# Kernel optimization log

Hardware: AMD Instinct MI355X
Metric: run time of the kernel (lower is better)

Reference implementation:

```python
import jax, jax.numpy as jnp
import numpy as np

ROPE_BASE = 10000.0

def rope_tables(n, r):
    inv = 1.0 / (ROPE_BASE ** (jnp.arange(0, r, 2, dtype=jnp.float32) / r))  # [r/2]
    ang = jnp.arange(n, dtype=jnp.float32)[:, None] * inv[None, :]           # [n, r/2]
    cos = jnp.concatenate([jnp.cos(ang), jnp.cos(ang)], axis=-1)             # [n, r]
    sin = jnp.concatenate([jnp.sin(ang), jnp.sin(ang)], axis=-1)
    return cos, sin

def apply_rope(x, cos, sin):
    # x: [B, H, T, r]; cos/sin: [T, r]
    half = x.shape[-1] // 2
    x_rot = jnp.concatenate([-x[..., half:], x[..., :half]], axis=-1)
    return x * cos + x_rot * sin

def setup_inputs() -> dict:
    key = jax.random.key(0)
    ks = jax.random.split(key, 8)
    B, S, L = 2, 1024, 1024
    dim_q, h, k, d_c, d_cq, r = 2048, 16, 128, 512, 1536, 64
    w = 0.02  # weight scale to keep activations numerically tame
    return {
        'hidden_q': jax.random.normal(ks[0], (B, S, dim_q), jnp.float32),
        'kv_c':     jax.random.normal(ks[1], (B, L, d_c), jnp.float32),
        'Wq':       jax.random.normal(ks[2], (h * k, dim_q), jnp.float32) * w,
        'w_kc_q':   jax.random.normal(ks[3], (h, k, d_cq), jnp.float32) * w,
        'W_qr':     jax.random.normal(ks[4], (h, d_cq, r), jnp.float32) * (w / np.sqrt(r)),
        'W_kr':     jax.random.normal(ks[5], (h, d_c, r), jnp.float32) * w,
        'w_kc_kv':  jax.random.normal(ks[6], (h, k, d_c), jnp.float32) * w,
        'Wo':       jax.random.normal(ks[7], (dim_q, h * k), jnp.float32) * w,
    }

def reference(hidden_q, kv_c, Wq, w_kc_q, W_qr, W_kr, w_kc_kv, Wo):
    B, S, _ = hidden_q.shape
    L = kv_c.shape[1]
    h, k, _ = w_kc_q.shape
    r = W_qr.shape[-1]
    # q projection: [B,S,h,k]
    q_hk = (hidden_q @ Wq.T).reshape(B, S, h, k)
    # low-rank expand to q-compressed space then retrieval space
    q_big = jnp.einsum('bshk,hkq->bshq', q_hk, w_kc_q)          # [B,S,h,d_cq]
    q_r = jnp.einsum('bshq,hqr->bhsr', q_big, W_qr)             # [B,h,S,r]
    k_r = jnp.einsum('bld,hdr->bhlr', kv_c, W_kr)               # [B,h,L,r]
    cos_S, sin_S = rope_tables(S, r)
    cos_L, sin_L = rope_tables(L, r)
    q_r = apply_rope(q_r, cos_S, sin_S)
    k_r = apply_rope(k_r, cos_L, sin_L)
    # attention in retrieval space, values are compressed kv (shared across heads)
    scores = jnp.einsum('bhsr,bhlr->bhsl', q_r, k_r)            # scale baked into W_qr
    attn = jax.nn.softmax(scores, axis=-1)
    ctx_c = jnp.einsum('bhsl,bld->bhsd', attn, kv_c)            # [B,h,S,d_c]
    # decompress per head: w_kc_kv is [h,k,d_c]
    ctx_lat = jnp.einsum('bhsd,hkd->bshk', ctx_c, w_kc_kv).reshape(B, S, h * k)
    return ctx_lat @ Wo.T
```

## Files before the change

kernel.cpp:

```cpp
#include <hip/hip_runtime.h>
#include <math.h>
#include <stdint.h>


typedef __attribute__((ext_vector_type(8))) short short8;
typedef __attribute__((ext_vector_type(4))) float f32x4;

#define GLOAD16(gsrc, ldst)                                                            \
  __builtin_amdgcn_global_load_lds((const __attribute__((address_space(1))) void*)(gsrc), \
                                   (__attribute__((address_space(3))) void*)(ldst), 16, 0, 0)

__device__ inline uint16_t f2b(float x) {
  uint32_t u = __builtin_bit_cast(uint32_t, x);
  u += 0x7fff + ((u >> 16) & 1);
  return (uint16_t)(u >> 16);
}
__device__ inline float b2f(uint16_t b) {
  uint32_t u = ((uint32_t)b) << 16;
  return __builtin_bit_cast(float, u);
}
__device__ inline uint32_t cvtpk_bf16(float lo, float hi) {
  uint32_t d;
  asm("v_cvt_pk_bf16_f32 %0, %1, %2" : "=v"(d) : "v"(lo), "v"(hi));
  return d;
}

__global__ __launch_bounds__(256) void prep_kernel(
    const float* __restrict__ s0, uint16_t* __restrict__ t0, const float* __restrict__ s1,
    uint16_t* __restrict__ t1, const float* __restrict__ s2, uint16_t* __restrict__ t2,
    const float* __restrict__ s3, uint16_t* __restrict__ t3, const float* __restrict__ s4,
    uint16_t* __restrict__ t4, float* __restrict__ cosK, float* __restrict__ sinK,
    float* __restrict__ cosQ, float* __restrict__ sinQ, const float* __restrict__ Wq,
    uint16_t* __restrict__ WqT, const float* __restrict__ W_qr, uint16_t* __restrict__ WqrT,
    const float* __restrict__ W_kr, uint16_t* __restrict__ WkrT) {
  __shared__ float t[32][33];
  int bid = blockIdx.x;
  if (bid >= 6912) {
    int tb = bid - 6912;
    const float* src;
    uint16_t* dst;
    int R, C, r0, c0;
    if (tb < 4096) {
      src = Wq; dst = WqT; R = 2048; C = 2048;
      r0 = (tb & 63) * 32; c0 = (tb >> 6) * 32;
    } else if (tb < 5632) {
      int b = tb - 4096;
      int z = b / 96, rem = b % 96;
      src = W_qr + (size_t)z * 98304; dst = WqrT + (size_t)z * 98304;
      R = 1536; C = 64;
      r0 = (rem >> 1) * 32; c0 = (rem & 1) * 32;
    } else {
      int b = tb - 5632;
      int z = b / 32, rem = b % 32;
      src = W_kr + (size_t)z * 32768; dst = WkrT + (size_t)z * 32768;
      R = 512; C = 64;
      r0 = (rem >> 1) * 32; c0 = (rem & 1) * 32;
    }
    int tr = threadIdx.x >> 5, tc = threadIdx.x & 31;
#pragma unroll
    for (int i = 0; i < 4; ++i) t[tr + i * 8][tc] = src[(size_t)(r0 + tr + i * 8) * C + c0 + tc];
    __syncthreads();
#pragma unroll
    for (int i = 0; i < 4; ++i)
      dst[(size_t)(c0 + tr + i * 8) * R + r0 + tc] = f2b(t[tc][tr + i * 8]);
    return;
  }
  if (bid >= 6656) {
    const float LOG2E = 1.44269504088896341f;
    int idx = (bid - 6656) * 256 + threadIdx.x;
    int s = idx >> 6, j = idx & 63;
    int i = j & 31;
    float inv = powf(10000.0f, -(float)(2 * i) / 64.0f);
    float ang = (float)s * inv;
    float c = cosf(ang), sn = sinf(ang);
    cosK[idx] = c;
    sinK[idx] = sn;
    cosQ[idx] = c * LOG2E;
    sinQ[idx] = sn * LOG2E;
    return;
  }
  const float* s;
  uint16_t* tt;
  int off;
  if (bid < 2048) { s = s0; tt = t0; off = bid; }
  else if (bid < 2560) { s = s1; tt = t1; off = bid - 2048; }
  else if (bid < 3072) { s = s2; tt = t2; off = bid - 2560; }
  else if (bid < 5120) { s = s3; tt = t3; off = bid - 3072; }
  else { s = s4; tt = t4; off = bid - 5120; }
  int i = off * 256 + threadIdx.x;
  const float4* s4v = (const float4*)s;
  float4 a = s4v[i * 2], b = s4v[i * 2 + 1];
  union {
    uint16_t u[8];
    uint4 v;
  } o;
  o.u[0] = f2b(a.x); o.u[1] = f2b(a.y); o.u[2] = f2b(a.z); o.u[3] = f2b(a.w);
  o.u[4] = f2b(b.x); o.u[5] = f2b(b.y); o.u[6] = f2b(b.z); o.u[7] = f2b(b.w);
  ((uint4*)tt)[i] = o.v;
}

template <int BM, int EPI, int SPLITK = 1>
__global__ __launch_bounds__(256) void gemm_mfma_kernel(const uint16_t* __restrict__ A,
                                                        const uint16_t* __restrict__ Bt,
                                                        void* __restrict__ Cv, int K, int lda,
                                                        int ldb, int ldc, int aZ, int bZ,
                                                        int cZ) {
  constexpr int MT = BM / 32;
  __shared__ __align__(16) uint16_t As[2][BM * 64];
  __shared__ __align__(16) uint16_t Bs[2][128 * 64];
  int z = blockIdx.z;
  if (SPLITK > 1) {
    int zh = z / SPLITK, zk = z % SPLITK;
    A += (size_t)zh * aZ + (size_t)zk * K;
    Bt += (size_t)zh * bZ + (size_t)zk * K;
  } else {
    A += (size_t)z * aZ;
    Bt += (size_t)z * bZ;
  }
  int m0 = blockIdx.x * BM, n0 = blockIdx.y * 128;
  int tid = threadIdx.x;
  int wave = tid >> 6, lane = tid & 63;
  int wm = wave >> 1, wn = wave & 1;
  int rS = lane >> 3, sl = lane & 7;
  int lr = lane >> 4, lc = lane & 15;

  auto stage = [&](int k0, int buf) {
#pragma unroll
    for (int i = 0; i < MT; ++i) {
      int idx = wave * MT + i;
      int row = idx * 8 + rS;
      GLOAD16(A + (size_t)(m0 + row) * lda + k0 + ((sl ^ (row & 7)) << 3),
              (uint8_t*)As[buf] + idx * 1024);
    }
#pragma unroll
    for (int i = 0; i < 4; ++i) {
      int idx = wave * 4 + i;
      int row = idx * 8 + rS;
      GLOAD16(Bt + (size_t)(n0 + row) * ldb + k0 + ((sl ^ (row & 7)) << 3),
              (uint8_t*)Bs[buf] + idx * 1024);
    }
  };

  f32x4 acc[MT][4] = {};
  stage(0, 0);
  int cur = 0;
  for (int k0 = 0; k0 < K; k0 += 64) {
    __syncthreads();
    if (k0 + 64 < K) stage(k0 + 64, cur ^ 1);
    short8 af[MT][2], bf[4][2];
#pragma unroll
    for (int t = 0; t < MT; ++t)
#pragma unroll
      for (int ks = 0; ks < 2; ++ks) {
        int slot = ks * 4 + lr;
        int ra = wm * (BM / 2) + t * 16 + lc;
        af[t][ks] =
            *(const short8*)((const uint8_t*)As[cur] + ra * 128 + ((slot ^ (ra & 7)) << 4));
      }
#pragma unroll
    for (int t = 0; t < 4; ++t)
#pragma unroll
      for (int ks = 0; ks < 2; ++ks) {
        int slot = ks * 4 + lr;
        int rb = wn * 64 + t * 16 + lc;
        bf[t][ks] =
            *(const short8*)((const uint8_t*)Bs[cur] + rb * 128 + ((slot ^ (rb & 7)) << 4));
      }
    __builtin_amdgcn_s_setprio(1);
#pragma unroll
    for (int mt = 0; mt < MT; ++mt)
#pragma unroll
      for (int nt = 0; nt < 4; ++nt) {
        acc[mt][nt] =
            __builtin_amdgcn_mfma_f32_16x16x32_bf16(af[mt][0], bf[nt][0], acc[mt][nt], 0, 0, 0);
        acc[mt][nt] =
            __builtin_amdgcn_mfma_f32_16x16x32_bf16(af[mt][1], bf[nt][1], acc[mt][nt], 0, 0, 0);
      }
    __builtin_amdgcn_s_setprio(0);
    cur ^= 1;
  }
#pragma unroll
  for (int mt = 0; mt < MT; ++mt)
#pragma unroll
    for (int nt = 0; nt < 4; ++nt)
#pragma unroll
      for (int r = 0; r < 4; ++r) {
        int m = m0 + wm * (BM / 2) + mt * 16 + lr * 4 + r;
        int n = n0 + wn * 64 + nt * 16 + lc;
        float v = acc[mt][nt][r];
        if (EPI == 0)
          ((float*)Cv)[(size_t)z * cZ + (size_t)m * ldc + n] = v;
        else
          ((uint16_t*)Cv)[(size_t)z * cZ + (size_t)m * ldc + n] = f2b(v);
      }
}

__global__ __launch_bounds__(256) void fold2_kernel(const float* __restrict__ tmp1,
                                                    const uint16_t* __restrict__ WqT,
                                                    uint16_t* __restrict__ WfoldT) {
  __shared__ __align__(16) uint16_t As[2][64 * 64];
  __shared__ __align__(16) uint16_t Bs[2][128 * 64];
  int z = blockIdx.z;
  int n0 = blockIdx.y * 128;
  const uint16_t* Bt = WqT + z * 128;
  int tid = threadIdx.x;
  int wave = tid >> 6, lane = tid & 63;
  int wm = wave >> 1, wn = wave & 1;
  int rS = lane >> 3, sl = lane & 7;
  int lr = lane >> 4, lc = lane & 15;

  {
    int row = tid >> 2;
    int kbase = (tid & 3) * 32;
    const float* tp = tmp1 + (size_t)z * 32768 + row * 128;
#pragma unroll
    for (int c = 0; c < 8; ++c) {
      int k4 = kbase + c * 4;
      float4 s = *(const float4*)(tp + k4);
      float4 s1 = *(const float4*)(tp + 8192 + k4);
      float4 s2 = *(const float4*)(tp + 16384 + k4);
      float4 s3 = *(const float4*)(tp + 24576 + k4);
      s.x = ((s.x + s1.x) + s2.x) + s3.x;
      s.y = ((s.y + s1.y) + s2.y) + s3.y;
      s.z = ((s.z + s1.z) + s2.z) + s3.z;
      s.w = ((s.w + s1.w) + s2.w) + s3.w;
      uint32_t lo = cvtpk_bf16(s.x, s.y);
      uint32_t hi = cvtpk_bf16(s.z, s.w);
      int buf = k4 >> 6, kl = k4 & 63;
      int slot = kl >> 3;
      uint32_t addr = row * 128 + ((slot ^ (row & 7)) << 4) + (kl & 7) * 2;
      *(uint32_t*)((uint8_t*)As[buf] + addr) = lo;
      *(uint32_t*)((uint8_t*)As[buf] + addr + 4) = hi;
    }
  }

  auto stageB = [&](int k0, int buf) {
#pragma unroll
    for (int i = 0; i < 4; ++i) {
      int idx = wave * 4 + i;
      int row = idx * 8 + rS;
      GLOAD16(Bt + (size_t)(n0 + row) * 2048 + k0 + ((sl ^ (row & 7)) << 3),
              (uint8_t*)Bs[buf] + idx * 1024);
    }
  };

  f32x4 acc[2][4] = {};
  stageB(0, 0);
  int cur = 0;
  for (int k0 = 0; k0 < 128; k0 += 64) {
    __syncthreads();
    if (k0 + 64 < 128) stageB(64, 1);
    short8 af[2][2], bf[4][2];
#pragma unroll
    for (int t = 0; t < 2; ++t)
#pragma unroll
      for (int ks = 0; ks < 2; ++ks) {
        int slot = ks * 4 + lr;
        int ra = wm * 32 + t * 16 + lc;
        af[t][ks] =
            *(const short8*)((const uint8_t*)As[cur] + ra * 128 + ((slot ^ (ra & 7)) << 4));
      }
#pragma unroll
    for (int t = 0; t < 4; ++t)
#pragma unroll
      for (int ks = 0; ks < 2; ++ks) {
        int slot = ks * 4 + lr;
        int rb = wn * 64 + t * 16 + lc;
        bf[t][ks] =
            *(const short8*)((const uint8_t*)Bs[cur] + rb * 128 + ((slot ^ (rb & 7)) << 4));
      }
    __builtin_amdgcn_s_setprio(1);
#pragma unroll
    for (int mt = 0; mt < 2; ++mt)
#pragma unroll
      for (int nt = 0; nt < 4; ++nt) {
        acc[mt][nt] =
            __builtin_amdgcn_mfma_f32_16x16x32_bf16(af[mt][0], bf[nt][0], acc[mt][nt], 0, 0, 0);
        acc[mt][nt] =
            __builtin_amdgcn_mfma_f32_16x16x32_bf16(af[mt][1], bf[nt][1], acc[mt][nt], 0, 0, 0);
      }
    __builtin_amdgcn_s_setprio(0);
    cur ^= 1;
  }
#pragma unroll
  for (int mt = 0; mt < 2; ++mt)
#pragma unroll
    for (int nt = 0; nt < 4; ++nt)
#pragma unroll
      for (int r = 0; r < 4; ++r) {
        int m = wm * 32 + mt * 16 + lr * 4 + r;
        int n = n0 + wn * 64 + nt * 16 + lc;
        WfoldT[(size_t)z * 131072 + (size_t)m * 2048 + n] = f2b(acc[mt][nt][r]);
      }
}

__global__ __launch_bounds__(256) void gemm_triple_kernel(
    const uint16_t* __restrict__ hqb, const uint16_t* __restrict__ WfoldT,
    uint16_t* __restrict__ qrb, const uint16_t* __restrict__ kvb,
    const uint16_t* __restrict__ WkrT, uint16_t* __restrict__ krb,
    const uint16_t* __restrict__ wkvb, uint16_t* __restrict__ VhT,
    const float* __restrict__ cosQ, const float* __restrict__ sinQ,
    const float* __restrict__ cosK, const float* __restrict__ sinK) {
  __shared__ __align__(16) uint16_t As[2][64 * 64];
  __shared__ __align__(16) uint16_t Bs[2][128 * 64];
  int bx = blockIdx.x, byr = blockIdx.y;
  const uint16_t *A, *Bt;
  uint16_t* Cv;
  const float *rc, *rs;
  int K, lda, ldb, n0, mode;
  if (byr < 8) {
    A = hqb; Bt = WfoldT; Cv = qrb; K = 2048; lda = 2048; ldb = 2048;
    n0 = byr * 128; mode = 0; rc = cosQ; rs = sinQ;
  } else if (byr < 16) {
    A = kvb; Bt = WkrT; Cv = krb; K = 512; lda = 512; ldb = 512;
    n0 = (byr - 8) * 128; mode = 0; rc = cosK; rs = sinK;
  } else {
    A = kvb; Bt = wkvb; Cv = VhT; K = 512; lda = 512; ldb = 512;
    n0 = (byr - 16) * 128; mode = 1; rc = nullptr; rs = nullptr;
  }
  int m0 = bx * 64;
  int tid = threadIdx.x;
  int wave = tid >> 6, lane = tid & 63;
  int wm = wave >> 1, wn = wave & 1;
  int rS = lane >> 3, sl = lane & 7;
  int lr = lane >> 4, lc = lane & 15;

  auto stage = [&](int k0, int buf) {
#pragma unroll
    for (int i = 0; i < 2; ++i) {
      int idx = wave * 2 + i;
      int row = idx * 8 + rS;
      GLOAD16(A + (size_t)(m0 + row) * lda + k0 + ((sl ^ (row & 7)) << 3),
              (uint8_t*)As[buf] + idx * 1024);
    }
#pragma unroll
    for (int i = 0; i < 4; ++i) {
      int idx = wave * 4 + i;
      int row = idx * 8 + rS;
      GLOAD16(Bt + (size_t)(n0 + row) * ldb + k0 + ((sl ^ (row & 7)) << 3),
              (uint8_t*)Bs[buf] + idx * 1024);
    }
  };

  f32x4 acc[2][4] = {};
  stage(0, 0);
  int cur = 0;
  for (int k0 = 0; k0 < K; k0 += 64) {
    __syncthreads();
    if (k0 + 64 < K) stage(k0 + 64, cur ^ 1);
    short8 af[2][2], bf[4][2];
#pragma unroll
    for (int t = 0; t < 2; ++t)
#pragma unroll
      for (int ks = 0; ks < 2; ++ks) {
        int slot = ks * 4 + lr;
        int ra = wm * 32 + t * 16 + lc;
        af[t][ks] =
            *(const short8*)((const uint8_t*)As[cur] + ra * 128 + ((slot ^ (ra & 7)) << 4));
      }
#pragma unroll
    for (int t = 0; t < 4; ++t)
#pragma unroll
      for (int ks = 0; ks < 2; ++ks) {
        int slot = ks * 4 + lr;
        int rb = wn * 64 + t * 16 + lc;
        bf[t][ks] =
            *(const short8*)((const uint8_t*)Bs[cur] + rb * 128 + ((slot ^ (rb & 7)) << 4));
      }
    __builtin_amdgcn_s_setprio(1);
#pragma unroll
    for (int mt = 0; mt < 2; ++mt)
#pragma unroll
      for (int nt = 0; nt < 4; ++nt) {
        acc[mt][nt] =
            __builtin_amdgcn_mfma_f32_16x16x32_bf16(af[mt][0], bf[nt][0], acc[mt][nt], 0, 0, 0);
        acc[mt][nt] =
            __builtin_amdgcn_mfma_f32_16x16x32_bf16(af[mt][1], bf[nt][1], acc[mt][nt], 0, 0, 0);
      }
    __builtin_amdgcn_s_setprio(0);
    cur ^= 1;
  }
  if (mode == 0) {
#pragma unroll
    for (int mt = 0; mt < 2; ++mt)
#pragma unroll
      for (int nt = 0; nt < 4; ++nt)
#pragma unroll
        for (int r = 0; r < 4; ++r) {
          int m = m0 + wm * 32 + mt * 16 + lr * 4 + r;
          int n = n0 + wn * 64 + nt * 16 + lc;
          int pos = m & 1023, j = n & 63;
          float x = acc[mt][nt][r];
          float prt = acc[mt][nt ^ 2][r];
          float rot = (nt & 2) ? prt : -prt;
          float v = fmaf(x, rc[pos * 64 + j], rot * rs[pos * 64 + j]);
          Cv[(size_t)m * 1024 + n] = f2b(v);
        }
  } else {
#pragma unroll
    for (int mt = 0; mt < 2; ++mt)
#pragma unroll
      for (int nt = 0; nt < 4; ++nt)
#pragma unroll
        for (int r = 0; r < 4; ++r) {
          int m = m0 + wm * 32 + mt * 16 + lr * 4 + r;
          int n = n0 + wn * 64 + nt * 16 + lc;
          Cv[((size_t)((m >> 10) * 2048 + n)) * 1024 + (m & 1023)] = f2b(acc[mt][nt][r]);
        }
  }
}

__global__ __launch_bounds__(512, 2) void flash3_kernel(const uint16_t* __restrict__ qrb,
                                                        const uint16_t* __restrict__ krb,
                                                        const uint16_t* __restrict__ VhT,
                                                        uint16_t* __restrict__ ctxlatb) {
  __shared__ __align__(16) uint8_t lds[67584];
  int bh = blockIdx.x;
  int b = bh >> 4, h = bh & 15;
  int s0 = blockIdx.y * 128;
  int tid = threadIdx.x, wave = tid >> 6, lane = tid & 63;
  int lr = lane >> 4, lc = lane & 15;
  int rS = lane >> 3, sl = lane & 7;

  uint8_t* Ps = lds + 49152 + wave * 2304;

  const uint16_t* qrow = qrb + (size_t)(b * 1024 + s0 + wave * 16 + lc) * 1024 + h * 64;
  short8 qa[2];
  qa[0] = *(const short8*)(qrow + lr * 8);
  qa[1] = *(const short8*)(qrow + 32 + lr * 8);

  float l_run = 0.f;
  f32x4 o[8] = {};

  uint8_t* psW = Ps + lc * 144 + lr * 8;
  const uint8_t* psR = Ps + lc * 144 + lr * 16;

  const uint16_t* krbase = krb + (size_t)(b * 1024) * 1024 + h * 64;
  const uint16_t* vtbase = VhT + (size_t)(b * 2048 + h * 128) * 1024;

  auto stageKV = [&](int l0, int buf) {
#pragma unroll
    for (int i = 0; i < 3; ++i) {
      int g = wave * 3 + i;
      if (g < 8) {
        int row = g * 8 + rS;
        GLOAD16(krbase + (size_t)(l0 + row) * 1024 + ((sl ^ (row & 7)) << 3),
                lds + buf * 8192 + g * 1024);
      } else {
        int v = g - 8;
        int row = v * 8 + rS;
        GLOAD16(vtbase + (size_t)row * 1024 + l0 + ((sl ^ (row & 7)) << 3),
                lds + 16384 + buf * 16384 + v * 1024);
      }
    }
  };

  stageKV(0, 0);
  int cur = 0;
  for (int t = 0; t < 16; ++t) {
    __syncthreads();
    if (t < 15) stageKV((t + 1) * 64, cur ^ 1);
    const uint8_t* Ks = lds + cur * 8192;
    const uint8_t* Vs = lds + 16384 + cur * 16384;

    f32x4 sc[4];
    __builtin_amdgcn_s_setprio(1);
#pragma unroll
    for (int nt = 0; nt < 4; ++nt) {
      int rowk = nt * 16 + lc;
      short8 kb0 = *(const short8*)(Ks + rowk * 128 + ((lr ^ (rowk & 7)) << 4));
      short8 kb1 = *(const short8*)(Ks + rowk * 128 + (((4 + lr) ^ (rowk & 7)) << 4));
      f32x4 z = {};
      z = __builtin_amdgcn_mfma_f32_16x16x32_bf16(kb0, qa[0], z, 0, 0, 0);
      sc[nt] = __builtin_amdgcn_mfma_f32_16x16x32_bf16(kb1, qa[1], z, 0, 0, 0);
    }
    __builtin_amdgcn_s_setprio(0);

    float ps = 0.f;
#pragma unroll
    for (int nt = 0; nt < 4; ++nt) {
#pragma unroll
      for (int rp = 0; rp < 2; ++rp) {
        float p0 = exp2f(sc[nt][rp * 2] - 8.0f);
        float p1 = exp2f(sc[nt][rp * 2 + 1] - 8.0f);
        ps += p0 + p1;
        *(uint32_t*)(psW + nt * 32 + rp * 4) = cvtpk_bf16(p0, p1);
      }
    }
    l_run += ps;

    short8 pa[2];
    pa[0] = *(const short8*)(psR);
    pa[1] = *(const short8*)(psR + 64);
    __builtin_amdgcn_s_setprio(1);
#pragma unroll
    for (int nt = 0; nt < 8; ++nt) {
      int rowv = nt * 16 + lc;
      short8 vb0 = *(const short8*)(Vs + rowv * 128 + ((lr ^ (rowv & 7)) << 4));
      short8 vb1 = *(const short8*)(Vs + rowv * 128 + (((4 + lr) ^ (rowv & 7)) << 4));
      o[nt] = __builtin_amdgcn_mfma_f32_16x16x32_bf16(pa[0], vb0, o[nt], 0, 0, 0);
      o[nt] = __builtin_amdgcn_mfma_f32_16x16x32_bf16(pa[1], vb1, o[nt], 0, 0, 0);
    }
    __builtin_amdgcn_s_setprio(0);
    cur ^= 1;
  }

  l_run += __shfl_xor(l_run, 16);
  l_run += __shfl_xor(l_run, 32);
  float li[4];
#pragma unroll
  for (int r = 0; r < 4; ++r) li[r] = 1.0f / __shfl(l_run, lr * 4 + r);
  uint16_t* orow = ctxlatb + (size_t)(b * 1024 + s0 + wave * 16) * 2048 + h * 128;
#pragma unroll
  for (int nt = 0; nt < 8; ++nt)
#pragma unroll
    for (int r = 0; r < 4; ++r)
      orow[(size_t)(lr * 4 + r) * 2048 + nt * 16 + lc] = f2b(o[nt][r] * li[r]);
}

extern "C" void kernel_launch(void* const* d_in, const int* in_sizes, int n_in,
                              void* d_out, int out_size, void* d_ws, size_t ws_size,
                              hipStream_t stream) {
  const float* hidden_q = (const float*)d_in[0];
  const float* kv_c = (const float*)d_in[1];
  const float* Wq = (const float*)d_in[2];
  const float* w_kc_q = (const float*)d_in[3];
  const float* W_qr = (const float*)d_in[4];
  const float* W_kr = (const float*)d_in[5];
  const float* w_kc_kv = (const float*)d_in[6];
  const float* Wo = (const float*)d_in[7];
  float* out = (float*)d_out;

  const size_t MB = 1024 * 1024;
  uint8_t* base = (uint8_t*)d_ws;
  uint16_t* Wob = (uint16_t*)(base + 0 * MB);
  uint16_t* qrb = (uint16_t*)(base + 8 * MB);
  uint16_t* krb = (uint16_t*)(base + 12 * MB);
  uint16_t* VhT = (uint16_t*)(base + 16 * MB);
  uint16_t* ctxlatb = (uint16_t*)(base + 24 * MB);
  float* cosK = (float*)(base + 32 * MB);
  float* sinK = (float*)(base + 32 * MB + 262144);
  float* cosQ = (float*)(base + 32 * MB + 524288);
  float* sinQ = (float*)(base + 32 * MB + 786432);
  uint16_t* hqb = (uint16_t*)(base + 33 * MB);
  uint16_t* kvb = (uint16_t*)(base + 41 * MB);
  uint16_t* wkvb = (uint16_t*)(base + 43 * MB);
  uint16_t* WqT = (uint16_t*)(base + 45 * MB);
  uint16_t* WqrT = (uint16_t*)(base + 53 * MB);
  uint16_t* wkcqb = (uint16_t*)(base + 56 * MB);
  float* tmp1 = (float*)(base + 62 * MB);
  uint16_t* WkrT = (uint16_t*)(base + 64 * MB + 262144);

  prep_kernel<<<dim3(13056), dim3(256), 0, stream>>>(
      hidden_q, hqb, kv_c, kvb, w_kc_kv, wkvb, Wo, Wob, w_kc_q, wkcqb, cosK, sinK, cosQ, sinQ, Wq,
      WqT, (const float*)W_qr, WqrT, (const float*)W_kr, WkrT);
  gemm_mfma_kernel<64, 0, 4><<<dim3(1, 1, 64), dim3(256), 0, stream>>>(
      WqrT, wkcqb, tmp1, 384, 1536, 1536, 128, 98304, 196608, 8192);
  uint16_t* WfoldT = wkcqb;
  fold2_kernel<<<dim3(1, 16, 16), dim3(256), 0, stream>>>(tmp1, WqT, WfoldT);
  gemm_triple_kernel<<<dim3(32, 32), dim3(256), 0, stream>>>(
      hqb, WfoldT, qrb, kvb, WkrT, krb, wkvb, VhT, cosQ, sinQ, cosK, sinK);
  flash3_kernel<<<dim3(32, 8), dim3(512), 0, stream>>>(qrb, krb, VhT, ctxlatb);
  gemm_mfma_kernel<64, 0><<<dim3(32, 16), dim3(256), 0, stream>>>(ctxlatb, Wob, out, 2048, 2048,
                                                                  2048, 2048, 0, 0, 0);
}
```

Measured before the change: 129.0 us.

## Add swizzled output GEMM, deepen split-K fold, pack bf16 conversion in prep

Replaces the final output projection with a dedicated GEMM that uses a blockwise tile swizzle for L2 locality and raised wave priority around the MFMA section. Raises the split-K factor of the W_qr fold GEMM from 4 to 8 so more blocks run in parallel, with fold2 now summing 8 partials. The workspace for tmp1 grows to hold them, so WkrT moves further out. Also swaps scalar bf16 rounding in the prep kernel for packed hardware conversion instructions.

Measured after the change: 133.5 us. 3.6% more time.

```diff
diff --git a/kernel.cpp b/kernel.cpp
--- a/kernel.cpp
+++ b/kernel.cpp
@@ -14,10 +14,6 @@
   uint32_t u = __builtin_bit_cast(uint32_t, x);
   u += 0x7fff + ((u >> 16) & 1);
   return (uint16_t)(u >> 16);
-}
-__device__ inline float b2f(uint16_t b) {
-  uint32_t u = ((uint32_t)b) << 16;
-  return __builtin_bit_cast(float, u);
 }
 __device__ inline uint32_t cvtpk_bf16(float lo, float hi) {
   uint32_t d;
@@ -90,13 +86,12 @@
   int i = off * 256 + threadIdx.x;
   const float4* s4v = (const float4*)s;
   float4 a = s4v[i * 2], b = s4v[i * 2 + 1];
-  union {
-    uint16_t u[8];
-    uint4 v;
-  } o;
-  o.u[0] = f2b(a.x); o.u[1] = f2b(a.y); o.u[2] = f2b(a.z); o.u[3] = f2b(a.w);
-  o.u[4] = f2b(b.x); o.u[5] = f2b(b.y); o.u[6] = f2b(b.z); o.u[7] = f2b(b.w);
-  ((uint4*)tt)[i] = o.v;
+  uint4 v;
+  v.x = cvtpk_bf16(a.x, a.y);
+  v.y = cvtpk_bf16(a.z, a.w);
+  v.z = cvtpk_bf16(b.x, b.y);
+  v.w = cvtpk_bf16(b.z, b.w);
+  ((uint4*)tt)[i] = v;
 }
 
 template <int BM, int EPI, int SPLITK = 1>
@@ -195,6 +190,87 @@
       }
 }
 
+__global__ __launch_bounds__(256) void gemm_out_kernel(const uint16_t* __restrict__ A,
+                                                       const uint16_t* __restrict__ Bt,
+                                                       float* __restrict__ C) {
+  __shared__ __align__(16) uint16_t As[2][64 * 64];
+  __shared__ __align__(16) uint16_t Bs[2][128 * 64];
+  int lin = blockIdx.x + 32 * blockIdx.y;
+  int swz = (lin & 7) * 64 + (lin >> 3);
+  int m0 = (swz & 31) * 64, n0 = (swz >> 5) * 128;
+  int tid = threadIdx.x;
+  int wave = tid >> 6, lane = tid & 63;
+  int wm = wave >> 1, wn = wave & 1;
+  int rS = lane >> 3, sl = lane & 7;
+  int lr = lane >> 4, lc = lane & 15;
+
+  auto stage = [&](int k0, int buf) {
+#pragma unroll
+    for (int i = 0; i < 2; ++i) {
+      int idx = wave * 2 + i;
+      int row = idx * 8 + rS;
+      GLOAD16(A + (size_t)(m0 + row) * 2048 + k0 + ((sl ^ (row & 7)) << 3),
+              (uint8_t*)As[buf] + idx * 1024);
+    }
+#pragma unroll
+    for (int i = 0; i < 4; ++i) {
+      int idx = wave * 4 + i;
+      int row = idx * 8 + rS;
+      GLOAD16(Bt + (size_t)(n0 + row) * 2048 + k0 + ((sl ^ (row & 7)) << 3),
+              (uint8_t*)Bs[buf] + idx * 1024);
+    }
+  };
+
+  f32x4 acc[2][4] = {};
+  stage(0, 0);
+  int cur = 0;
+  for (int k0 = 0; k0 < 2048; k0 += 64) {
+    __syncthreads();
+    if (k0 + 64 < 2048) stage(k0 + 64, cur ^ 1);
+    short8 af[2][2], bf[4][2];
+#pragma unroll
+    for (int t = 0; t < 2; ++t)
+#pragma unroll
+      for (int ks = 0; ks < 2; ++ks) {
+        int slot = ks * 4 + lr;
+        int ra = wm * 32 + t * 16 + lc;
+        af[t][ks] =
+            *(const short8*)((const uint8_t*)As[cur] + ra * 128 + ((slot ^ (ra & 7)) << 4));
+      }
+#pragma unroll
+    for (int t = 0; t < 4; ++t)
+#pragma unroll
+      for (int ks = 0; ks < 2; ++ks) {
+        int slot = ks * 4 + lr;
+        int rb = wn * 64 + t * 16 + lc;
+        bf[t][ks] =
+            *(const short8*)((const uint8_t*)Bs[cur] + rb * 128 + ((slot ^ (rb & 7)) << 4));
+      }
+    __builtin_amdgcn_s_setprio(1);
+#pragma unroll
+    for (int mt = 0; mt < 2; ++mt)
+#pragma unroll
+      for (int nt = 0; nt < 4; ++nt) {
+        acc[mt][nt] =
+            __builtin_amdgcn_mfma_f32_16x16x32_bf16(af[mt][0], bf[nt][0], acc[mt][nt], 0, 0, 0);
+        acc[mt][nt] =
+            __builtin_amdgcn_mfma_f32_16x16x32_bf16(af[mt][1], bf[nt][1], acc[mt][nt], 0, 0, 0);
+      }
+    __builtin_amdgcn_s_setprio(0);
+    cur ^= 1;
+  }
+#pragma unroll
+  for (int mt = 0; mt < 2; ++mt)
+#pragma unroll
+    for (int nt = 0; nt < 4; ++nt)
+#pragma unroll
+      for (int r = 0; r < 4; ++r) {
+        int m = m0 + wm * 32 + mt * 16 + lr * 4 + r;
+        int n = n0 + wn * 64 + nt * 16 + lc;
+        C[(size_t)m * 2048 + n] = acc[mt][nt][r];
+      }
+}
+
 __global__ __launch_bounds__(256) void fold2_kernel(const float* __restrict__ tmp1,
                                                     const uint16_t* __restrict__ WqT,
                                                     uint16_t* __restrict__ WfoldT) {
@@ -212,18 +288,19 @@
   {
     int row = tid >> 2;
     int kbase = (tid & 3) * 32;
-    const float* tp = tmp1 + (size_t)z * 32768 + row * 128;
+    const float* tp = tmp1 + (size_t)z * 65536 + row * 128;
 #pragma unroll
     for (int c = 0; c < 8; ++c) {
       int k4 = kbase + c * 4;
       float4 s = *(const float4*)(tp + k4);
-      float4 s1 = *(const float4*)(tp + 8192 + k4);
-      float4 s2 = *(const float4*)(tp + 16384 + k4);
-      float4 s3 = *(const float4*)(tp + 24576 + k4);
-      s.x = ((s.x + s1.x) + s2.x) + s3.x;
-      s.y = ((s.y + s1.y) + s2.y) + s3.y;
-      s.z = ((s.z + s1.z) + s2.z) + s3.z;
-      s.w = ((s.w + s1.w) + s2.w) + s3.w;
+#pragma unroll
+      for (int p = 1; p < 8; ++p) {
+        float4 sp = *(const float4*)(tp + p * 8192 + k4);
+        s.x += sp.x;
+        s.y += sp.y;
+        s.z += sp.z;
+        s.w += sp.w;
+      }
       uint32_t lo = cvtpk_bf16(s.x, s.y);
       uint32_t hi = cvtpk_bf16(s.z, s.w);
       int buf = k4 >> 6, kl = k4 & 63;
@@ -549,18 +626,17 @@
   uint16_t* WqrT = (uint16_t*)(base + 53 * MB);
   uint16_t* wkcqb = (uint16_t*)(base + 56 * MB);
   float* tmp1 = (float*)(base + 62 * MB);
-  uint16_t* WkrT = (uint16_t*)(base + 64 * MB + 262144);
+  uint16_t* WkrT = (uint16_t*)(base + 66 * MB);
 
   prep_kernel<<<dim3(13056), dim3(256), 0, stream>>>(
       hidden_q, hqb, kv_c, kvb, w_kc_kv, wkvb, Wo, Wob, w_kc_q, wkcqb, cosK, sinK, cosQ, sinQ, Wq,
       WqT, (const float*)W_qr, WqrT, (const float*)W_kr, WkrT);
-  gemm_mfma_kernel<64, 0, 4><<<dim3(1, 1, 64), dim3(256), 0, stream>>>(
-      WqrT, wkcqb, tmp1, 384, 1536, 1536, 128, 98304, 196608, 8192);
+  gemm_mfma_kernel<64, 0, 8><<<dim3(1, 1, 128), dim3(256), 0, stream>>>(
+      WqrT, wkcqb, tmp1, 192, 1536, 1536, 128, 98304, 196608, 8192);
   uint16_t* WfoldT = wkcqb;
   fold2_kernel<<<dim3(1, 16, 16), dim3(256), 0, stream>>>(tmp1, WqT, WfoldT);
   gemm_triple_kernel<<<dim3(32, 32), dim3(256), 0, stream>>>(
       hqb, WfoldT, qrb, kvb, WkrT, krb, wkvb, VhT, cosQ, sinQ, cosK, sinK);
   flash3_kernel<<<dim3(32, 8), dim3(512), 0, stream>>>(qrb, krb, VhT, ctxlatb);
-  gemm_mfma_kernel<64, 0><<<dim3(32, 16), dim3(256), 0, stream>>>(ctxlatb, Wob, out, 2048, 2048,
-                                                                  2048, 2048, 0, 0, 0);
-}
+  gemm_out_kernel<<<dim3(32, 16), dim3(256), 0, stream>>>(ctxlatb, Wob, out);
+}
```
